# Optimization experiments

Hardware: AMD Instinct MI355X
Metric: run time of the kernel (lower is better)

## Reference

```python
import jax, jax.numpy as jnp
import numpy as np

H = 8        # heads
DH = 64      # dim_head
IMG = 32     # image_size
KS = 5       # kernel_size (odd)
SCALE = DH ** -0.5


def _unfold(t, ks):
    # t: (b, c, Hp, Wp) already padded. Returns (b, c*ks*ks, Ho*Wo) with
    # channel-major layout (c outermost, then kh, kw) matching torch F.unfold.
    b, c, Hp, Wp = t.shape
    Ho, Wo = Hp - ks + 1, Wp - ks + 1
    pat = jnp.stack([t[:, :, i:i + Ho, j:j + Wo]
                     for i in range(ks) for j in range(ks)], axis=2)  # (b,c,ks*ks,Ho,Wo)
    return pat.reshape(b, c * ks * ks, Ho * Wo)


def setup_inputs() -> dict:
    key = jax.random.key(0)
    k1, k2, k3, k4 = jax.random.split(key, 4)
    b, n, dim, inner = 2, 1152, 512, 512
    x = jax.random.normal(k1, (b, n, dim), jnp.float32)
    w_qkv = jax.random.normal(k2, (dim, inner * 3), jnp.float32) * 0.02
    w_out = jax.random.normal(k3, (inner, dim), jnp.float32) * 0.02
    b_out = jax.random.normal(k4, (dim,), jnp.float32) * 0.02
    return {"x": x, "w_qkv": w_qkv, "w_out": w_out, "b_out": b_out}


def reference(x, w_qkv, w_out, b_out):
    b, n, dim = x.shape
    img_len = IMG * IMG
    text_len = n - img_len
    NEG = -jnp.finfo(x.dtype).max

    qkv = x @ w_qkv                                   # (b, n, 3*inner)
    q, k, v = jnp.split(qkv, 3, axis=-1)

    def to_heads(t):
        return t.reshape(b, n, H, DH).transpose(0, 2, 1, 3).reshape(b * H, n, DH)

    q = to_heads(q) * SCALE
    k = to_heads(k)
    v = to_heads(v)

    # faithful to source: text slice is t[:, img_seq_len:], image is t[:, -img_seq_len:]
    q_text, q_img = q[:, img_len:], q[:, -img_len:]
    k_text, k_img = k[:, img_len:], k[:, -img_len:]
    v_text, v_img = v[:, img_len:], v[:, -img_len:]

    # ---- text branch. NOTE: source uses non-inplace masked_fill, so the
    # causal mask has NO effect -> plain softmax (faithful reproduction).
    dots_text = jnp.einsum('bid,bjd->bij', q_text, k_text)
    attn_text = jax.nn.softmax(dots_text, axis=-1)
    out_text = jnp.einsum('bij,bjd->bid', attn_text, v_text)

    # ---- image branch: local window via unfold
    def to_loc(t):
        g = t.transpose(0, 2, 1).reshape(b * H, DH, IMG, IMG)
        p = KS // 2
        g = jnp.pad(g, ((0, 0), (0, 0), (p, p), (p, p)))
        u = _unfold(g, KS)  # (bh, DH*KS*KS, img_len), channel-major (d outer)
        # faithful to source rearrange 'b (j d) i -> b i j d' (j outermost),
        # which regroups the channel-major unfold output.
        return u.reshape(b * H, KS * KS, DH, img_len).transpose(0, 3, 1, 2)

    k_loc = to_loc(k_img)  # (bh, img_len, KS*KS, DH)
    v_loc = to_loc(v_img)

    dots_txt = jnp.einsum('bid,bjd->bij', q_img, k_text)     # (bh, img_len, text_len)
    dots_loc = jnp.einsum('bid,bijd->bij', q_img, k_loc)     # (bh, img_len, KS*KS)

    # per-query key index mask (padded positions get index img_len -> never masked)
    p = KS // 2
    idx = jnp.arange(img_len, dtype=jnp.float32).reshape(1, 1, IMG, IMG)
    idx = jnp.pad(idx, ((0, 0), (0, 0), (p, p), (p, p)), constant_values=float(img_len))
    kidx = _unfold(idx, KS).transpose(0, 2, 1)               # (1, img_len, KS*KS)
    qidx = jnp.arange(img_len, dtype=jnp.float32).reshape(1, -1, 1)
    mask_loc = qidx <= kidx                                  # faithful: keep q <= k
    dots_loc = jnp.where(mask_loc, dots_loc, NEG)

    dots_img = jnp.concatenate([dots_txt, dots_loc], axis=-1)
    attn_img = jax.nn.softmax(dots_img, axis=-1)
    out_img = (jnp.einsum('bij,bjd->bid', attn_img[..., :text_len], v_text)
               + jnp.einsum('bij,bijd->bid', attn_img[..., text_len:], v_loc))

    out = jnp.concatenate([out_text, out_img], axis=1)       # (bh, n, DH)
    out = out.reshape(b, H, n, DH).transpose(0, 2, 1, 3).reshape(b, n, H * DH)
    return out @ w_out + b_out
```

## Files before the change

kernel.cpp:

```cpp
#include <hip/hip_runtime.h>
#include <hip/hip_bf16.h>
#include <math.h>

#define NTOK 1152
#define DIM 512
#define NQKV 1536
#define DHEAD 64
#define NBH 16
#define TEXTN 128
#define IMGLEN 1024
#define SEG (NBH * NTOK * DHEAD)
#define THR 4.0f
#define STF 68
#define TSTATE_F (NBH * IMGLEN * STF)
#define LPAD 40

typedef __attribute__((ext_vector_type(8))) short bf16x8;
typedef __attribute__((ext_vector_type(4))) float f32x4;

__device__ __forceinline__ ushort f2bf(float f) {
    unsigned u = __float_as_uint(f);
    unsigned r = (u + 0x7FFFu + ((u >> 16) & 1u)) >> 16;
    return (ushort)r;
}
__device__ __forceinline__ float bf2f(ushort u) {
    return __uint_as_float(((unsigned)u) << 16);
}

__global__ __launch_bounds__(256) void prep_x_k(const float* __restrict__ X,
                                                ushort* __restrict__ xhi,
                                                ushort* __restrict__ xlo) {
    int i = (blockIdx.x * 256 + threadIdx.x) * 4;
    float4 v = *(const float4*)(X + i);
    ushort4 h, l;
    h.x = f2bf(v.x); l.x = f2bf(v.x - bf2f(h.x));
    h.y = f2bf(v.y); l.y = f2bf(v.y - bf2f(h.y));
    h.z = f2bf(v.z); l.z = f2bf(v.z - bf2f(h.z));
    h.w = f2bf(v.w); l.w = f2bf(v.w - bf2f(h.w));
    *(ushort4*)(xhi + i) = h;
    *(ushort4*)(xlo + i) = l;
}

__global__ __launch_bounds__(256) void prep_wt_k(const float* __restrict__ W,
                                                 ushort* __restrict__ thi,
                                                 ushort* __restrict__ tlo,
                                                 int K, int N) {
    __shared__ float tile[32][33];
    const int bx = blockIdx.x, by = blockIdx.y;
    const int c = threadIdx.x & 31, r8 = threadIdx.x >> 5;
#pragma unroll
    for (int i = 0; i < 4; ++i) {
        int rr = r8 + i * 8;
        tile[rr][c] = W[(size_t)(by * 32 + rr) * N + bx * 32 + c];
    }
    __syncthreads();
#pragma unroll
    for (int i = 0; i < 4; ++i) {
        int rr = r8 + i * 8;
        float v = tile[c][rr];
        size_t o = (size_t)(bx * 32 + rr) * K + by * 32 + c;
        ushort h = f2bf(v);
        thi[o] = h;
        tlo[o] = f2bf(v - bf2f(h));
    }
}

__global__ __launch_bounds__(256) void gemm_qkv_mfma(const ushort* __restrict__ xhi,
                                                     const ushort* __restrict__ xlo,
                                                     const ushort* __restrict__ wthi,
                                                     const ushort* __restrict__ wtlo,
                                                     float* __restrict__ qh,
                                                     float* __restrict__ kh,
                                                     float* __restrict__ vh) {
    __shared__ __align__(16) ushort Ah[128 * LPAD], Al[128 * LPAD];
    __shared__ __align__(16) ushort Bh[64 * LPAD], Bl[64 * LPAD];
    const int tid = threadIdx.x;
    const int lane = tid & 63;
    const int w = tid >> 6;
    const int wm = w >> 1, wn = w & 1;
    const int row0 = blockIdx.y * 128;
    const int col0 = blockIdx.x * 64;

    f32x4 acc[4][2];
#pragma unroll
    for (int a = 0; a < 4; ++a)
#pragma unroll
        for (int b = 0; b < 2; ++b) acc[a][b] = (f32x4){0.f, 0.f, 0.f, 0.f};

    const int arow = tid >> 1;
    const int akb = (tid & 1) * 16;
    const int brow = tid >> 2;
    const int bkb = (tid & 3) * 8;
    const int kf = (lane >> 4) * 8;
    const int lr = lane & 15;

    for (int k0 = 0; k0 < DIM; k0 += 32) {
        {
            const size_t g = (size_t)(row0 + arow) * DIM + k0 + akb;
            *(bf16x8*)&Ah[arow * LPAD + akb] = *(const bf16x8*)(xhi + g);
            *(bf16x8*)&Ah[arow * LPAD + akb + 8] = *(const bf16x8*)(xhi + g + 8);
            *(bf16x8*)&Al[arow * LPAD + akb] = *(const bf16x8*)(xlo + g);
            *(bf16x8*)&Al[arow * LPAD + akb + 8] = *(const bf16x8*)(xlo + g + 8);
        }
        {
            const size_t g = (size_t)(col0 + brow) * DIM + k0 + bkb;
            *(bf16x8*)&Bh[brow * LPAD + bkb] = *(const bf16x8*)(wthi + g);
            *(bf16x8*)&Bl[brow * LPAD + bkb] = *(const bf16x8*)(wtlo + g);
        }
        __syncthreads();
        bf16x8 ah[4], al[4], bh[2], bl[2];
#pragma unroll
        for (int mi = 0; mi < 4; ++mi) {
            int rr = wm * 64 + mi * 16 + lr;
            ah[mi] = *(const bf16x8*)&Ah[rr * LPAD + kf];
            al[mi] = *(const bf16x8*)&Al[rr * LPAD + kf];
        }
#pragma unroll
        for (int ni = 0; ni < 2; ++ni) {
            int rr = wn * 32 + ni * 16 + lr;
            bh[ni] = *(const bf16x8*)&Bh[rr * LPAD + kf];
            bl[ni] = *(const bf16x8*)&Bl[rr * LPAD + kf];
        }
#pragma unroll
        for (int mi = 0; mi < 4; ++mi)
#pragma unroll
            for (int ni = 0; ni < 2; ++ni) {
                acc[mi][ni] = __builtin_amdgcn_mfma_f32_16x16x32_bf16(ah[mi], bh[ni], acc[mi][ni], 0, 0, 0);
                acc[mi][ni] = __builtin_amdgcn_mfma_f32_16x16x32_bf16(ah[mi], bl[ni], acc[mi][ni], 0, 0, 0);
                acc[mi][ni] = __builtin_amdgcn_mfma_f32_16x16x32_bf16(al[mi], bh[ni], acc[mi][ni], 0, 0, 0);
            }
        __syncthreads();
    }

    const int which = col0 >> 9;
    const int hh = (col0 & 511) >> 6;
    const float scale = (which == 0) ? 0.125f : 1.f;
    float* dst = (which == 0) ? qh : ((which == 1) ? kh : vh);
#pragma unroll
    for (int mi = 0; mi < 4; ++mi)
#pragma unroll
        for (int ni = 0; ni < 2; ++ni)
#pragma unroll
            for (int j = 0; j < 4; ++j) {
                int r = row0 + wm * 64 + mi * 16 + (lane >> 4) * 4 + j;
                int b_i = r / NTOK, tok = r - b_i * NTOK;
                int d = wn * 32 + ni * 16 + (lane & 15);
                dst[((size_t)(b_i * 8 + hh) * NTOK + tok) * DHEAD + d] = acc[mi][ni][j] * scale;
            }
}

__global__ __launch_bounds__(128) void attn_text_k(const float* __restrict__ qh,
                                                   const float* __restrict__ kh,
                                                   const float* __restrict__ vh,
                                                   ushort* __restrict__ ahi,
                                                   ushort* __restrict__ alo,
                                                   float* __restrict__ tstate) {
    const int bh = blockIdx.x / 36;
    const int c = blockIdx.x % 36;
    const bool is_img = (c < 32);
    const int wave = threadIdx.x >> 6;
    const int lane = threadIdx.x & 63;
    const int qsub = lane & 31, h = lane >> 5;
    const int hb = h * 32;
    const int qq = (is_img ? c : (c - 32)) * 32 + qsub;
    const int token = is_img ? (TEXTN + qq) : (IMGLEN + qq);
    const float* ktext = kh + (size_t)(bh * NTOK + IMGLEN) * DHEAD;
    const float* vtext = vh + (size_t)(bh * NTOK + IMGLEN) * DHEAD;

    float q[32];
    {
        const float* qp = qh + ((size_t)(bh * NTOK + token)) * DHEAD + hb;
#pragma unroll
        for (int e4 = 0; e4 < 8; ++e4) {
            float4 v4 = *(const float4*)(qp + e4 * 4);
            q[e4 * 4] = v4.x; q[e4 * 4 + 1] = v4.y; q[e4 * 4 + 2] = v4.z; q[e4 * 4 + 3] = v4.w;
        }
    }
    float out[32];
#pragma unroll
    for (int e = 0; e < 32; ++e) out[e] = 0.f;
    float m = -1e30f, l = 0.f;

    const int j0 = wave * 64;
#pragma unroll 2
    for (int j = j0; j < j0 + 64; ++j) {
        const float* kr = ktext + j * DHEAD + hb;
        float p0 = 0.f, p1 = 0.f, p2 = 0.f, p3 = 0.f;
#pragma unroll
        for (int e4 = 0; e4 < 8; ++e4) {
            float4 kv = *(const float4*)(kr + e4 * 4);
            p0 += q[e4 * 4] * kv.x;
            p1 += q[e4 * 4 + 1] * kv.y;
            p2 += q[e4 * 4 + 2] * kv.z;
            p3 += q[e4 * 4 + 3] * kv.w;
        }
        float part = (p0 + p1) + (p2 + p3);
        float dot = part + __shfl_xor(part, 32);
        if (dot > m + THR) {
            float cc = __expf(m - dot);
            l *= cc;
#pragma unroll
            for (int e = 0; e < 32; ++e) out[e] *= cc;
            m = dot;
        }
        float p = __expf(dot - m);
        l += p;
        const float* vr = vtext + j * DHEAD + hb;
#pragma unroll
        for (int e4 = 0; e4 < 8; ++e4) {
            float4 vv = *(const float4*)(vr + e4 * 4);
            out[e4 * 4] += p * vv.x;
            out[e4 * 4 + 1] += p * vv.y;
            out[e4 * 4 + 2] += p * vv.z;
            out[e4 * 4 + 3] += p * vv.w;
        }
    }

    __shared__ float mbuf[2][64];
    __shared__ float lbuf[2][64];
    __shared__ float ob[64][36];
    mbuf[wave][lane] = m;
    lbuf[wave][lane] = l;
    __syncthreads();
    float M = fmaxf(mbuf[0][lane], mbuf[1][lane]);
    float cw = __expf(m - M);
    if (wave == 1) {
#pragma unroll
        for (int e4 = 0; e4 < 8; ++e4) {
            float4 o;
            o.x = cw * out[e4 * 4]; o.y = cw * out[e4 * 4 + 1];
            o.z = cw * out[e4 * 4 + 2]; o.w = cw * out[e4 * 4 + 3];
            *(float4*)&ob[lane][e4 * 4] = o;
        }
        lbuf[1][lane] = cw * l;
    }
    __syncthreads();
    if (wave == 0) {
        float lt = cw * l + lbuf[1][lane];
#pragma unroll
        for (int e = 0; e < 32; ++e) out[e] = cw * out[e] + ob[lane][e];
        if (is_img) {
            float* st = tstate + ((size_t)(bh * IMGLEN + qq)) * STF;
#pragma unroll
            for (int e4 = 0; e4 < 8; ++e4) {
                float4 o;
                o.x = out[e4 * 4]; o.y = out[e4 * 4 + 1];
                o.z = out[e4 * 4 + 2]; o.w = out[e4 * 4 + 3];
                *(float4*)(st + hb + e4 * 4) = o;
            }
            if (h == 0) { st[64] = M; st[65] = lt; }
        } else {
            float inv = 1.f / lt;
            size_t base = ((size_t)(bh * NTOK + qq)) * DHEAD + hb;
#pragma unroll
            for (int e4 = 0; e4 < 8; ++e4) {
                float v0 = out[e4 * 4] * inv, v1 = out[e4 * 4 + 1] * inv;
                float v2 = out[e4 * 4 + 2] * inv, v3 = out[e4 * 4 + 3] * inv;
                ushort4 oh, ol;
                oh.x = f2bf(v0); ol.x = f2bf(v0 - bf2f(oh.x));
                oh.y = f2bf(v1); ol.y = f2bf(v1 - bf2f(oh.y));
                oh.z = f2bf(v2); ol.z = f2bf(v2 - bf2f(oh.z));
                oh.w = f2bf(v3); ol.w = f2bf(v3 - bf2f(oh.w));
                *(ushort4*)(ahi + base + e4 * 4) = oh;
                *(ushort4*)(alo + base + e4 * 4) = ol;
            }
        }
    }
}

template <int W>
__device__ inline void loc_dots(const float* __restrict__ kimg, int y, int x,
                                const float (&q)[64], float (&sd)[25]) {
#pragma unroll
    for (int t = 0; t < 25; ++t) {
        const int ny = y + t / 5 - 2;
        const int nx = x + t % 5 - 2;
        if (ny >= 0 && ny < 32 && nx >= 0 && nx < 32) {
            const float* kp = kimg + (size_t)(ny * 32 + nx) * DHEAD + W * 16;
#pragma unroll
            for (int g = 0; g < 4; ++g) {
                float4 kv = *(const float4*)(kp + g * 4);
                float ke[4] = {kv.x, kv.y, kv.z, kv.w};
#pragma unroll
                for (int e = 0; e < 4; ++e) {
                    const int d = W * 16 + g * 4 + e;
                    const int id2 = d * 25 + t;
                    sd[id2 >> 6] += q[id2 & 63] * ke[e];
                }
            }
        }
    }
}

template <int W>
__device__ inline void loc_pv(const float* __restrict__ vimg, int y, int x,
                              const float (&p)[25], float (&po)[64]) {
#pragma unroll
    for (int t = 0; t < 25; ++t) {
        const int ny = y + t / 5 - 2;
        const int nx = x + t % 5 - 2;
        if (ny >= 0 && ny < 32 && nx >= 0 && nx < 32) {
            const float* vp = vimg + (size_t)(ny * 32 + nx) * DHEAD + W * 16;
#pragma unroll
            for (int g = 0; g < 4; ++g) {
                float4 vv = *(const float4*)(vp + g * 4);
                float ve[4] = {vv.x, vv.y, vv.z, vv.w};
#pragma unroll
                for (int e = 0; e < 4; ++e) {
                    const int d = W * 16 + g * 4 + e;
                    const int id2 = d * 25 + t;
                    po[id2 & 63] += p[id2 >> 6] * ve[e];
                }
            }
        }
    }
}

__global__ __launch_bounds__(256) void attn_img_k(const float* __restrict__ qh,
                                                  const float* __restrict__ kh,
                                                  const float* __restrict__ vh,
                                                  ushort* __restrict__ ahi,
                                                  ushort* __restrict__ alo,
                                                  const float* __restrict__ tstate) {
    __shared__ float sdb[4][64][27];
    __shared__ float pob[2][64][68];
    const int bh = blockIdx.x >> 4;
    const int qtile = (blockIdx.x & 15) << 6;
    const int wave = threadIdx.x >> 6;
    const int lane = threadIdx.x & 63;
    const int qq = qtile + lane;
    const int y = qq >> 5, x = qq & 31;
    const float* kimg = kh + (size_t)(bh * NTOK + TEXTN) * DHEAD;
    const float* vimg = vh + (size_t)(bh * NTOK + TEXTN) * DHEAD;
    const float* st = tstate + ((size_t)(bh * IMGLEN + qq)) * STF;

    float sd[25];
#pragma unroll
    for (int j = 0; j < 25; ++j) sd[j] = 0.f;
    {
        float q[64];
        const float* qp = qh + ((size_t)(bh * NTOK + TEXTN + qq)) * DHEAD;
#pragma unroll
        for (int g = 0; g < 16; ++g) {
            float4 v4 = *(const float4*)(qp + g * 4);
            q[g * 4] = v4.x; q[g * 4 + 1] = v4.y; q[g * 4 + 2] = v4.z; q[g * 4 + 3] = v4.w;
        }
        if (wave == 0) loc_dots<0>(kimg, y, x, q, sd);
        else if (wave == 1) loc_dots<1>(kimg, y, x, q, sd);
        else if (wave == 2) loc_dots<2>(kimg, y, x, q, sd);
        else loc_dots<3>(kimg, y, x, q, sd);
    }
#pragma unroll
    for (int j = 0; j < 25; ++j) sdb[wave][lane][j] = sd[j];
    __syncthreads();

    float p[25];
#pragma unroll
    for (int j = 0; j < 25; ++j)
        p[j] = (sdb[0][lane][j] + sdb[1][lane][j]) + (sdb[2][lane][j] + sdb[3][lane][j]);
    float m = st[64], l = st[65];
    float mloc = -1e30f;
#pragma unroll
    for (int j = 0; j < 25; ++j) {
        const int my = y + j / 5 - 2;
        const int mx = x + j % 5 - 2;
        bool inb = (my >= 0 && my < 32 && mx >= 0 && mx < 32);
        bool keep = inb ? (qq <= my * 32 + mx) : true;
        p[j] = keep ? p[j] : -1e30f;
        mloc = fmaxf(mloc, p[j]);
    }
    const float M = fmaxf(m, mloc);
    const float cc = __expf(m - M);
    l *= cc;
#pragma unroll
    for (int j = 0; j < 25; ++j) {
        p[j] = __expf(p[j] - M);
        l += p[j];
    }
    const float inv = 1.f / l;

    float po[64];
#pragma unroll
    for (int o = 0; o < 64; ++o) po[o] = 0.f;
    if (wave == 0) loc_pv<0>(vimg, y, x, p, po);
    else if (wave == 1) loc_pv<1>(vimg, y, x, p, po);
    else if (wave == 2) loc_pv<2>(vimg, y, x, p, po);
    else loc_pv<3>(vimg, y, x, p, po);

    if (wave < 2) {
#pragma unroll
        for (int o = 0; o < 64; ++o) pob[wave][lane][o] = po[o];
    }
    __syncthreads();
    if (wave >= 2) {
#pragma unroll
        for (int o = 0; o < 64; ++o) pob[wave - 2][lane][o] += po[o];
    }
    __syncthreads();

    {
        const float* stq = st + wave * 16;
        size_t base = ((size_t)(bh * NTOK + TEXTN + qq)) * DHEAD + wave * 16;
#pragma unroll
        for (int g = 0; g < 4; ++g) {
            float4 tv = *(const float4*)(stq + g * 4);
            float4 a0 = *(const float4*)&pob[0][lane][wave * 16 + g * 4];
            float4 a1 = *(const float4*)&pob[1][lane][wave * 16 + g * 4];
            float v0 = (a0.x + a1.x + cc * tv.x) * inv;
            float v1 = (a0.y + a1.y + cc * tv.y) * inv;
            float v2 = (a0.z + a1.z + cc * tv.z) * inv;
            float v3 = (a0.w + a1.w + cc * tv.w) * inv;
            ushort4 oh, ol;
            oh.x = f2bf(v0); ol.x = f2bf(v0 - bf2f(oh.x));
            oh.y = f2bf(v1); ol.y = f2bf(v1 - bf2f(oh.y));
            oh.z = f2bf(v2); ol.z = f2bf(v2 - bf2f(oh.z));
            oh.w = f2bf(v3); ol.w = f2bf(v3 - bf2f(oh.w));
            *(ushort4*)(ahi + base + g * 4) = oh;
            *(ushort4*)(alo + base + g * 4) = ol;
        }
    }
}

__global__ __launch_bounds__(256) void gemm_out_mfma(const ushort* __restrict__ ahi,
                                                     const ushort* __restrict__ alo,
                                                     const ushort* __restrict__ wthi,
                                                     const ushort* __restrict__ wtlo,
                                                     const float* __restrict__ bias,
                                                     float* __restrict__ Y) {
    __shared__ __align__(16) ushort Ah[128 * LPAD], Al[128 * LPAD];
    __shared__ __align__(16) ushort Bh[64 * LPAD], Bl[64 * LPAD];
    const int tid = threadIdx.x;
    const int lane = tid & 63;
    const int w = tid >> 6;
    const int wm = w >> 1, wn = w & 1;
    const int row0 = blockIdx.y * 128;
    const int col0 = blockIdx.x * 64;

    f32x4 acc[4][2];
#pragma unroll
    for (int a = 0; a < 4; ++a)
#pragma unroll
        for (int b = 0; b < 2; ++b) acc[a][b] = (f32x4){0.f, 0.f, 0.f, 0.f};

    const int arow = tid >> 1;
    const int akb = (tid & 1) * 16;
    const int brow = tid >> 2;
    const int bkb = (tid & 3) * 8;
    const int kf = (lane >> 4) * 8;
    const int lr = lane & 15;

    const int ar = row0 + arow;
    const int a_bi = ar / NTOK;
    const int a_tok = ar - a_bi * NTOK;

    for (int k0 = 0; k0 < DIM; k0 += 32) {
        {
            const int kg = k0 + akb;
            const int hh = kg >> 6, d0 = kg & 63;
            const size_t g = ((size_t)(a_bi * 8 + hh) * NTOK + a_tok) * DHEAD + d0;
            *(bf16x8*)&Ah[arow * LPAD + akb] = *(const bf16x8*)(ahi + g);
            *(bf16x8*)&Ah[arow * LPAD + akb + 8] = *(const bf16x8*)(ahi + g + 8);
            *(bf16x8*)&Al[arow * LPAD + akb] = *(const bf16x8*)(alo + g);
            *(bf16x8*)&Al[arow * LPAD + akb + 8] = *(const bf16x8*)(alo + g + 8);
        }
        {
            const size_t g = (size_t)(col0 + brow) * DIM + k0 + bkb;
            *(bf16x8*)&Bh[brow * LPAD + bkb] = *(const bf16x8*)(wthi + g);
            *(bf16x8*)&Bl[brow * LPAD + bkb] = *(const bf16x8*)(wtlo + g);
        }
        __syncthreads();
        bf16x8 ah[4], al[4], bh[2], bl[2];
#pragma unroll
        for (int mi = 0; mi < 4; ++mi) {
            int rr = wm * 64 + mi * 16 + lr;
            ah[mi] = *(const bf16x8*)&Ah[rr * LPAD + kf];
            al[mi] = *(const bf16x8*)&Al[rr * LPAD + kf];
        }
#pragma unroll
        for (int ni = 0; ni < 2; ++ni) {
            int rr = wn * 32 + ni * 16 + lr;
            bh[ni] = *(const bf16x8*)&Bh[rr * LPAD + kf];
            bl[ni] = *(const bf16x8*)&Bl[rr * LPAD + kf];
        }
#pragma unroll
        for (int mi = 0; mi < 4; ++mi)
#pragma unroll
            for (int ni = 0; ni < 2; ++ni) {
                acc[mi][ni] = __builtin_amdgcn_mfma_f32_16x16x32_bf16(ah[mi], bh[ni], acc[mi][ni], 0, 0, 0);
                acc[mi][ni] = __builtin_amdgcn_mfma_f32_16x16x32_bf16(ah[mi], bl[ni], acc[mi][ni], 0, 0, 0);
                acc[mi][ni] = __builtin_amdgcn_mfma_f32_16x16x32_bf16(al[mi], bh[ni], acc[mi][ni], 0, 0, 0);
            }
        __syncthreads();
    }

#pragma unroll
    for (int mi = 0; mi < 4; ++mi)
#pragma unroll
        for (int ni = 0; ni < 2; ++ni) {
            int cidx = col0 + wn * 32 + ni * 16 + (lane & 15);
            float bv = bias[cidx];
#pragma unroll
            for (int j = 0; j < 4; ++j) {
                int r = row0 + wm * 64 + mi * 16 + (lane >> 4) * 4 + j;
                Y[(size_t)r * DIM + cidx] = acc[mi][ni][j] + bv;
            }
        }
}

extern "C" void kernel_launch(void* const* d_in, const int* in_sizes, int n_in,
                              void* d_out, int out_size, void* d_ws, size_t ws_size,
                              hipStream_t stream) {
    const float* x = (const float*)d_in[0];
    const float* w_qkv = (const float*)d_in[1];
    const float* w_out = (const float*)d_in[2];
    const float* b_out = (const float*)d_in[3];
    float* Y = (float*)d_out;
    float* ws = (float*)d_ws;
    float* qh = ws;
    float* kh = ws + (size_t)SEG;
    float* vh = ws + 2 * (size_t)SEG;
    float* tstate = ws + 3 * (size_t)SEG;
    ushort* xhi = (ushort*)(ws + 3 * (size_t)SEG + TSTATE_F);
    ushort* xlo = xhi + (size_t)SEG;
    ushort* ahi = xhi;
    ushort* alo = xlo;
    ushort* wqthi = xlo + (size_t)SEG;
    ushort* wqtlo = wqthi + (size_t)DIM * NQKV;
    ushort* wothi = wqtlo + (size_t)DIM * NQKV;
    ushort* wotlo = wothi + (size_t)DIM * DIM;

    hipLaunchKernelGGL(prep_x_k, dim3(SEG / 1024), dim3(256), 0, stream, x, xhi, xlo);
    hipLaunchKernelGGL(prep_wt_k, dim3(NQKV / 32, DIM / 32), dim3(256), 0, stream,
                       w_qkv, wqthi, wqtlo, DIM, NQKV);
    hipLaunchKernelGGL(prep_wt_k, dim3(DIM / 32, DIM / 32), dim3(256), 0, stream,
                       w_out, wothi, wotlo, DIM, DIM);
    hipLaunchKernelGGL(gemm_qkv_mfma, dim3(NQKV / 64, 2304 / 128), dim3(256), 0, stream,
                       xhi, xlo, wqthi, wqtlo, qh, kh, vh);
    hipLaunchKernelGGL(attn_text_k, dim3(NBH * 36), dim3(128), 0, stream,
                       qh, kh, vh, ahi, alo, tstate);
    hipLaunchKernelGGL(attn_img_k, dim3(NBH * 16), dim3(256), 0, stream,
                       qh, kh, vh, ahi, alo, tstate);
    hipLaunchKernelGGL(gemm_out_mfma, dim3(DIM / 64, 2304 / 128), dim3(256), 0, stream,
                       ahi, alo, wothi, wotlo, b_out, Y);
}
```

Before: 148.4 us.

## Compute text-key attention with split-bf16 MFMA instead of scalar online softmax

Replaces the scalar per-thread online-softmax text attention kernel with an MFMA-based kernel that computes full 128-key score tiles using hi/lo bf16 split products, does a one-pass softmax, and multiplies P by V via MFMA through shared memory. The QKV GEMM epilogue now also emits bf16 hi/lo copies of Q, text K, and transposed text V for this kernel. The aim is to move the text-branch FLOPs onto matrix cores. In exchange the GEMM epilogue does more scattered narrow stores and uses extra workspace, and precision drops slightly from the three-term bf16 split.

After: 132.3 us. -10.9%, faster.

```diff
diff --git a/kernel.cpp b/kernel.cpp
--- a/kernel.cpp
+++ b/kernel.cpp
@@ -10,10 +10,10 @@
 #define TEXTN 128
 #define IMGLEN 1024
 #define SEG (NBH * NTOK * DHEAD)
-#define THR 4.0f
 #define STF 68
 #define TSTATE_F (NBH * IMGLEN * STF)
 #define LPAD 40
+#define KTSZ (NBH * TEXTN * DHEAD)
 
 typedef __attribute__((ext_vector_type(8))) short bf16x8;
 typedef __attribute__((ext_vector_type(4))) float f32x4;
@@ -71,7 +71,13 @@
                                                      const ushort* __restrict__ wtlo,
                                                      float* __restrict__ qh,
                                                      float* __restrict__ kh,
-                                                     float* __restrict__ vh) {
+                                                     float* __restrict__ vh,
+                                                     ushort* __restrict__ qhi,
+                                                     ushort* __restrict__ qlo,
+                                                     ushort* __restrict__ kthi,
+                                                     ushort* __restrict__ ktlo,
+                                                     ushort* __restrict__ vthi,
+                                                     ushort* __restrict__ vtlo) {
     __shared__ __align__(16) ushort Ah[128 * LPAD], Al[128 * LPAD];
     __shared__ __align__(16) ushort Bh[64 * LPAD], Bl[64 * LPAD];
     const int tid = threadIdx.x;
@@ -145,125 +151,148 @@
                 int r = row0 + wm * 64 + mi * 16 + (lane >> 4) * 4 + j;
                 int b_i = r / NTOK, tok = r - b_i * NTOK;
                 int d = wn * 32 + ni * 16 + (lane & 15);
-                dst[((size_t)(b_i * 8 + hh) * NTOK + tok) * DHEAD + d] = acc[mi][ni][j] * scale;
-            }
-}
-
-__global__ __launch_bounds__(128) void attn_text_k(const float* __restrict__ qh,
-                                                   const float* __restrict__ kh,
-                                                   const float* __restrict__ vh,
-                                                   ushort* __restrict__ ahi,
-                                                   ushort* __restrict__ alo,
-                                                   float* __restrict__ tstate) {
-    const int bh = blockIdx.x / 36;
-    const int c = blockIdx.x % 36;
-    const bool is_img = (c < 32);
+                int bhi = b_i * 8 + hh;
+                float val = acc[mi][ni][j] * scale;
+                dst[((size_t)bhi * NTOK + tok) * DHEAD + d] = val;
+                if (which == 0) {
+                    size_t qo = ((size_t)bhi * NTOK + tok) * DHEAD + d;
+                    ushort h2 = f2bf(val);
+                    qhi[qo] = h2;
+                    qlo[qo] = f2bf(val - bf2f(h2));
+                } else if (tok >= IMGLEN) {
+                    int tr = tok - IMGLEN;
+                    ushort h2 = f2bf(val);
+                    ushort l2 = f2bf(val - bf2f(h2));
+                    if (which == 1) {
+                        size_t ko = ((size_t)bhi * TEXTN + tr) * DHEAD + d;
+                        kthi[ko] = h2; ktlo[ko] = l2;
+                    } else {
+                        size_t vo = ((size_t)bhi * DHEAD + d) * TEXTN + tr;
+                        vthi[vo] = h2; vtlo[vo] = l2;
+                    }
+                }
+            }
+}
+
+__global__ __launch_bounds__(256) void attn_text_mfma(const ushort* __restrict__ qhi,
+                                                      const ushort* __restrict__ qlo,
+                                                      const ushort* __restrict__ kthi,
+                                                      const ushort* __restrict__ ktlo,
+                                                      const ushort* __restrict__ vthi,
+                                                      const ushort* __restrict__ vtlo,
+                                                      ushort* __restrict__ ahi,
+                                                      ushort* __restrict__ alo,
+                                                      float* __restrict__ tstate) {
+    __shared__ __align__(16) ushort Phi[4][16][136];
+    __shared__ __align__(16) ushort Plo[4][16][136];
+    const int bh = blockIdx.x / 18;
+    const int tile = blockIdx.x % 18;
     const int wave = threadIdx.x >> 6;
     const int lane = threadIdx.x & 63;
-    const int qsub = lane & 31, h = lane >> 5;
-    const int hb = h * 32;
-    const int qq = (is_img ? c : (c - 32)) * 32 + qsub;
-    const int token = is_img ? (TEXTN + qq) : (IMGLEN + qq);
-    const float* ktext = kh + (size_t)(bh * NTOK + IMGLEN) * DHEAD;
-    const float* vtext = vh + (size_t)(bh * NTOK + IMGLEN) * DHEAD;
-
-    float q[32];
+    const int lr = lane & 15, lg = lane >> 4;
+    const int kf = lg * 8;
+    const int qrow0 = tile * 64 + wave * 16;
+    const int tok0 = (tile < 2 ? 1024 + tile * 64 : tile * 64) + wave * 16;
+
+    bf16x8 qah[2], qal[2];
     {
-        const float* qp = qh + ((size_t)(bh * NTOK + token)) * DHEAD + hb;
-#pragma unroll
-        for (int e4 = 0; e4 < 8; ++e4) {
-            float4 v4 = *(const float4*)(qp + e4 * 4);
-            q[e4 * 4] = v4.x; q[e4 * 4 + 1] = v4.y; q[e4 * 4 + 2] = v4.z; q[e4 * 4 + 3] = v4.w;
-        }
-    }
-    float out[32];
-#pragma unroll
-    for (int e = 0; e < 32; ++e) out[e] = 0.f;
-    float m = -1e30f, l = 0.f;
-
-    const int j0 = wave * 64;
-#pragma unroll 2
-    for (int j = j0; j < j0 + 64; ++j) {
-        const float* kr = ktext + j * DHEAD + hb;
-        float p0 = 0.f, p1 = 0.f, p2 = 0.f, p3 = 0.f;
-#pragma unroll
-        for (int e4 = 0; e4 < 8; ++e4) {
-            float4 kv = *(const float4*)(kr + e4 * 4);
-            p0 += q[e4 * 4] * kv.x;
-            p1 += q[e4 * 4 + 1] * kv.y;
-            p2 += q[e4 * 4 + 2] * kv.z;
-            p3 += q[e4 * 4 + 3] * kv.w;
-        }
-        float part = (p0 + p1) + (p2 + p3);
-        float dot = part + __shfl_xor(part, 32);
-        if (dot > m + THR) {
-            float cc = __expf(m - dot);
-            l *= cc;
-#pragma unroll
-            for (int e = 0; e < 32; ++e) out[e] *= cc;
-            m = dot;
-        }
-        float p = __expf(dot - m);
-        l += p;
-        const float* vr = vtext + j * DHEAD + hb;
-#pragma unroll
-        for (int e4 = 0; e4 < 8; ++e4) {
-            float4 vv = *(const float4*)(vr + e4 * 4);
-            out[e4 * 4] += p * vv.x;
-            out[e4 * 4 + 1] += p * vv.y;
-            out[e4 * 4 + 2] += p * vv.z;
-            out[e4 * 4 + 3] += p * vv.w;
-        }
-    }
-
-    __shared__ float mbuf[2][64];
-    __shared__ float lbuf[2][64];
-    __shared__ float ob[64][36];
-    mbuf[wave][lane] = m;
-    lbuf[wave][lane] = l;
+        const size_t qb = ((size_t)bh * NTOK + tok0 + lr) * DHEAD;
+#pragma unroll
+        for (int c = 0; c < 2; ++c) {
+            qah[c] = *(const bf16x8*)(qhi + qb + c * 32 + kf);
+            qal[c] = *(const bf16x8*)(qlo + qb + c * 32 + kf);
+        }
+    }
+    f32x4 s[8];
+#pragma unroll
+    for (int t = 0; t < 8; ++t) s[t] = (f32x4){0.f, 0.f, 0.f, 0.f};
+#pragma unroll
+    for (int t = 0; t < 8; ++t) {
+        const size_t kb = ((size_t)bh * TEXTN + t * 16 + lr) * DHEAD;
+#pragma unroll
+        for (int c = 0; c < 2; ++c) {
+            bf16x8 kbh = *(const bf16x8*)(kthi + kb + c * 32 + kf);
+            bf16x8 kbl = *(const bf16x8*)(ktlo + kb + c * 32 + kf);
+            s[t] = __builtin_amdgcn_mfma_f32_16x16x32_bf16(qah[c], kbh, s[t], 0, 0, 0);
+            s[t] = __builtin_amdgcn_mfma_f32_16x16x32_bf16(qah[c], kbl, s[t], 0, 0, 0);
+            s[t] = __builtin_amdgcn_mfma_f32_16x16x32_bf16(qal[c], kbh, s[t], 0, 0, 0);
+        }
+    }
+    float mx[4], sm[4];
+#pragma unroll
+    for (int r = 0; r < 4; ++r) {
+        float v = s[0][r];
+#pragma unroll
+        for (int t = 1; t < 8; ++t) v = fmaxf(v, s[t][r]);
+        mx[r] = v;
+    }
+#pragma unroll
+    for (int msk = 1; msk <= 8; msk <<= 1)
+#pragma unroll
+        for (int r = 0; r < 4; ++r) mx[r] = fmaxf(mx[r], __shfl_xor(mx[r], msk));
+#pragma unroll
+    for (int r = 0; r < 4; ++r) sm[r] = 0.f;
+#pragma unroll
+    for (int t = 0; t < 8; ++t)
+#pragma unroll
+        for (int r = 0; r < 4; ++r) {
+            float p = __expf(s[t][r] - mx[r]);
+            s[t][r] = p;
+            sm[r] += p;
+        }
+#pragma unroll
+    for (int msk = 1; msk <= 8; msk <<= 1)
+#pragma unroll
+        for (int r = 0; r < 4; ++r) sm[r] += __shfl_xor(sm[r], msk);
+#pragma unroll
+    for (int t = 0; t < 8; ++t)
+#pragma unroll
+        for (int r = 0; r < 4; ++r) {
+            float p = s[t][r];
+            ushort h = f2bf(p);
+            Phi[wave][lg * 4 + r][t * 16 + lr] = h;
+            Plo[wave][lg * 4 + r][t * 16 + lr] = f2bf(p - bf2f(h));
+        }
     __syncthreads();
-    float M = fmaxf(mbuf[0][lane], mbuf[1][lane]);
-    float cw = __expf(m - M);
-    if (wave == 1) {
-#pragma unroll
-        for (int e4 = 0; e4 < 8; ++e4) {
-            float4 o;
-            o.x = cw * out[e4 * 4]; o.y = cw * out[e4 * 4 + 1];
-            o.z = cw * out[e4 * 4 + 2]; o.w = cw * out[e4 * 4 + 3];
-            *(float4*)&ob[lane][e4 * 4] = o;
-        }
-        lbuf[1][lane] = cw * l;
-    }
-    __syncthreads();
-    if (wave == 0) {
-        float lt = cw * l + lbuf[1][lane];
-#pragma unroll
-        for (int e = 0; e < 32; ++e) out[e] = cw * out[e] + ob[lane][e];
-        if (is_img) {
-            float* st = tstate + ((size_t)(bh * IMGLEN + qq)) * STF;
-#pragma unroll
-            for (int e4 = 0; e4 < 8; ++e4) {
-                float4 o;
-                o.x = out[e4 * 4]; o.y = out[e4 * 4 + 1];
-                o.z = out[e4 * 4 + 2]; o.w = out[e4 * 4 + 3];
-                *(float4*)(st + hb + e4 * 4) = o;
-            }
-            if (h == 0) { st[64] = M; st[65] = lt; }
-        } else {
-            float inv = 1.f / lt;
-            size_t base = ((size_t)(bh * NTOK + qq)) * DHEAD + hb;
-#pragma unroll
-            for (int e4 = 0; e4 < 8; ++e4) {
-                float v0 = out[e4 * 4] * inv, v1 = out[e4 * 4 + 1] * inv;
-                float v2 = out[e4 * 4 + 2] * inv, v3 = out[e4 * 4 + 3] * inv;
-                ushort4 oh, ol;
-                oh.x = f2bf(v0); ol.x = f2bf(v0 - bf2f(oh.x));
-                oh.y = f2bf(v1); ol.y = f2bf(v1 - bf2f(oh.y));
-                oh.z = f2bf(v2); ol.z = f2bf(v2 - bf2f(oh.z));
-                oh.w = f2bf(v3); ol.w = f2bf(v3 - bf2f(oh.w));
-                *(ushort4*)(ahi + base + e4 * 4) = oh;
-                *(ushort4*)(alo + base + e4 * 4) = ol;
-            }
+    f32x4 o[4];
+#pragma unroll
+    for (int dt = 0; dt < 4; ++dt) o[dt] = (f32x4){0.f, 0.f, 0.f, 0.f};
+#pragma unroll
+    for (int c = 0; c < 4; ++c) {
+        bf16x8 pah = *(const bf16x8*)&Phi[wave][lr][c * 32 + kf];
+        bf16x8 pal = *(const bf16x8*)&Plo[wave][lr][c * 32 + kf];
+#pragma unroll
+        for (int dt = 0; dt < 4; ++dt) {
+            const size_t vb = ((size_t)bh * DHEAD + dt * 16 + lr) * TEXTN + c * 32 + kf;
+            bf16x8 vbh = *(const bf16x8*)(vthi + vb);
+            bf16x8 vbl = *(const bf16x8*)(vtlo + vb);
+            o[dt] = __builtin_amdgcn_mfma_f32_16x16x32_bf16(pah, vbh, o[dt], 0, 0, 0);
+            o[dt] = __builtin_amdgcn_mfma_f32_16x16x32_bf16(pah, vbl, o[dt], 0, 0, 0);
+            o[dt] = __builtin_amdgcn_mfma_f32_16x16x32_bf16(pal, vbh, o[dt], 0, 0, 0);
+        }
+    }
+    if (tile < 2) {
+#pragma unroll
+        for (int r = 0; r < 4; ++r) {
+            const int row = qrow0 + lg * 4 + r;
+            const float inv = 1.f / sm[r];
+            const size_t base = ((size_t)bh * NTOK + row) * DHEAD;
+#pragma unroll
+            for (int dt = 0; dt < 4; ++dt) {
+                float v = o[dt][r] * inv;
+                ushort h = f2bf(v);
+                ahi[base + dt * 16 + lr] = h;
+                alo[base + dt * 16 + lr] = f2bf(v - bf2f(h));
+            }
+        }
+    } else {
+#pragma unroll
+        for (int r = 0; r < 4; ++r) {
+            const int imgq = qrow0 - TEXTN + lg * 4 + r;
+            float* st = tstate + ((size_t)bh * IMGLEN + imgq) * STF;
+#pragma unroll
+            for (int dt = 0; dt < 4; ++dt) st[dt * 16 + lr] = o[dt][r];
+            if (lr == 0) { st[64] = mx[r]; st[65] = sm[r]; }
         }
     }
 }
@@ -528,6 +557,12 @@
     ushort* wqtlo = wqthi + (size_t)DIM * NQKV;
     ushort* wothi = wqtlo + (size_t)DIM * NQKV;
     ushort* wotlo = wothi + (size_t)DIM * DIM;
+    ushort* qhi = wotlo + (size_t)DIM * DIM;
+    ushort* qlo = qhi + (size_t)SEG;
+    ushort* kthi = qlo + (size_t)SEG;
+    ushort* ktlo = kthi + (size_t)KTSZ;
+    ushort* vthi = ktlo + (size_t)KTSZ;
+    ushort* vtlo = vthi + (size_t)KTSZ;
 
     hipLaunchKernelGGL(prep_x_k, dim3(SEG / 1024), dim3(256), 0, stream, x, xhi, xlo);
     hipLaunchKernelGGL(prep_wt_k, dim3(NQKV / 32, DIM / 32), dim3(256), 0, stream,
@@ -535,9 +570,10 @@
     hipLaunchKernelGGL(prep_wt_k, dim3(DIM / 32, DIM / 32), dim3(256), 0, stream,
                        w_out, wothi, wotlo, DIM, DIM);
     hipLaunchKernelGGL(gemm_qkv_mfma, dim3(NQKV / 64, 2304 / 128), dim3(256), 0, stream,
-                       xhi, xlo, wqthi, wqtlo, qh, kh, vh);
-    hipLaunchKernelGGL(attn_text_k, dim3(NBH * 36), dim3(128), 0, stream,
-                       qh, kh, vh, ahi, alo, tstate);
+                       xhi, xlo, wqthi, wqtlo, qh, kh, vh,
+                       qhi, qlo, kthi, ktlo, vthi, vtlo);
+    hipLaunchKernelGGL(attn_text_mfma, dim3(NBH * 18), dim3(256), 0, stream,
+                       qhi, qlo, kthi, ktlo, vthi, vtlo, ahi, alo, tstate);
     hipLaunchKernelGGL(attn_img_k, dim3(NBH * 16), dim3(256), 0, stream,
                        qh, kh, vh, ahi, alo, tstate);
     hipLaunchKernelGGL(gemm_out_mfma, dim3(DIM / 64, 2304 / 128), dim3(256), 0, stream,
```
